# Kernel tuning notes

Measured on AMD Instinct MI355X. Metric: run time of the kernel, lower is better.

Reference implementation:

```python
import jax, jax.numpy as jnp
import numpy as np

D_MODEL = 1024
N_HEADS = 16
D_K = D_MODEL // N_HEADS
MAX_REL = 128
SCALE = 1.0 / np.sqrt(D_K)
TEMP = 1.0


def setup_inputs() -> dict:
    key = jax.random.key(0)
    ks = jax.random.split(key, 12)
    B, S = 4, 1024
    inp = {
        "query": jax.random.normal(ks[0], (B, S, D_MODEL), jnp.float32),
        "key": jax.random.normal(ks[1], (B, S, D_MODEL), jnp.float32),
        "value": jax.random.normal(ks[2], (B, S, D_MODEL), jnp.float32),
        "mask": jnp.ones((B, S), jnp.int32),
        "w_q": jax.random.normal(ks[3], (D_MODEL, D_MODEL), jnp.float32) * 0.03,
        "b_q": jnp.zeros((D_MODEL,), jnp.float32),
        "w_k": jax.random.normal(ks[4], (D_MODEL, D_MODEL), jnp.float32) * 0.03,
        "b_k": jnp.zeros((D_MODEL,), jnp.float32),
        "w_v": jax.random.normal(ks[5], (D_MODEL, D_MODEL), jnp.float32) * 0.03,
        "b_v": jnp.zeros((D_MODEL,), jnp.float32),
        "w_o": jax.random.normal(ks[6], (D_MODEL, D_MODEL), jnp.float32) * 0.03,
        "b_o": jnp.zeros((D_MODEL,), jnp.float32),
        "rel_k": jax.random.normal(ks[7], (2 * MAX_REL + 1, D_K), jnp.float32),
        "rel_v": jax.random.normal(ks[8], (2 * MAX_REL + 1, D_K), jnp.float32),
    }
    return inp


def _relative_positions(seq_len):
    pos = jnp.arange(seq_len)
    rel = pos[None, :] - pos[:, None]  # [S, S]
    return jnp.clip(rel, -MAX_REL, MAX_REL) + MAX_REL


def reference(query, key, value, mask, w_q, b_q, w_k, b_k, w_v, b_v, w_o, b_o, rel_k, rel_v):
    B, S, _ = query.shape
    # projections (torch Linear: x @ W.T + b)
    Q = (query @ w_q.T + b_q).reshape(B, S, N_HEADS, D_K).transpose(0, 2, 1, 3)  # [B,H,S,d]
    K = (key @ w_k.T + b_k).reshape(B, S, N_HEADS, D_K).transpose(0, 2, 1, 3)
    V = (value @ w_v.T + b_v).reshape(B, S, N_HEADS, D_K).transpose(0, 2, 1, 3)

    scores = jnp.einsum("bhld,bhrd->bhlr", Q, K) * SCALE  # [B,H,S,S]

    rel_idx = _relative_positions(S)                      # [S,S] int
    rpk = rel_k[rel_idx]                                  # [S,S,d]
    scores = scores + jnp.einsum("bhld,lrd->bhlr", Q, rpk)

    scores = scores / TEMP
    m = mask[:, None, None, :]                            # [B,1,1,S]
    scores = jnp.where(m == 0, -1e9, scores)

    attn = jax.nn.softmax(scores, axis=-1)                # [B,H,S,S]
    context = jnp.einsum("bhlr,bhrd->bhld", attn, V)
    rpv = rel_v[rel_idx]                                  # [S,S,d]
    context = context + jnp.einsum("bhlr,lrd->bhld", attn, rpv)

    context = context.transpose(0, 2, 1, 3).reshape(B, S, D_MODEL)
    out = context @ w_o.T + b_o
    return out
```

## Files before the change

### kernel.cpp

```cpp
#include <hip/hip_runtime.h>
#include <hip/hip_bf16.h>

#define S_LEN  1024
#define DMODEL 1024
#define NHEADS 16
#define DK     64
#define SCALE  0.125f

typedef __bf16 bf16x8_t __attribute__((ext_vector_type(8)));
typedef __bf16 bf16x4_t __attribute__((ext_vector_type(4)));
typedef float  f32x4_t  __attribute__((ext_vector_type(4)));

#define MFMA16(A, B, C) __builtin_amdgcn_mfma_f32_16x16x32_bf16((A), (B), (C), 0, 0, 0)

__device__ __forceinline__ void async16(const void* g, void* l) {
    __builtin_amdgcn_global_load_lds(
        (const __attribute__((address_space(1))) unsigned int*)g,
        (__attribute__((address_space(3))) unsigned int*)l, 16, 0, 0);
}

__global__ __launch_bounds__(256) void cast_all_kernel(
    const float* __restrict__ q, const float* __restrict__ k, const float* __restrict__ v,
    const float* __restrict__ wq, const float* __restrict__ wk,
    const float* __restrict__ wv, const float* __restrict__ wo,
    const float* __restrict__ relk, const float* __restrict__ relv,
    __bf16* __restrict__ Xbf, __bf16* __restrict__ Wall,
    __bf16* __restrict__ relkp, __bf16* __restrict__ rvT,
    __bf16* __restrict__ Wqlo)
{
    const long i = (long)blockIdx.x * 256 + threadIdx.x;
    if (i < 3145728) {
        const int z   = (int)(i >> 20);
        const long rem = i & 1048575;
        const float4 s = ((const float4*)(z == 0 ? q : (z == 1 ? k : v)))[rem];
        bf16x4_t h;
        h[0] = (__bf16)s.x; h[1] = (__bf16)s.y; h[2] = (__bf16)s.z; h[3] = (__bf16)s.w;
        *(bf16x4_t*)(Xbf + ((size_t)z << 22) + rem * 4) = h;
    } else if (i < 3145728 + 1048576) {
        const long wi = i - 3145728;
        const int z   = (int)(wi >> 18);
        const long rem = wi & 262143;
        const float* src = (z == 0) ? wq : (z == 1) ? wk : (z == 2) ? wv : wo;
        const float4 s = ((const float4*)src)[rem];
        const float xs[4] = {s.x, s.y, s.z, s.w};
        bf16x4_t h;
        #pragma unroll
        for (int t = 0; t < 4; ++t) h[t] = (__bf16)xs[t];
        *(bf16x4_t*)(Wall + ((size_t)z << 20) + rem * 4) = h;
        if (z == 0) {
            bf16x4_t l;
            #pragma unroll
            for (int t = 0; t < 4; ++t) l[t] = (__bf16)(xs[t] - (float)h[t]);
            *(bf16x4_t*)(Wqlo + rem * 4) = l;
        }
    } else if (i < 3145728 + 1048576 + 4352) {
        const long ri = i - (3145728 + 1048576);
        const int j  = (int)(ri >> 4);
        const int d4 = (int)(ri & 15) * 4;
        bf16x4_t h, l;
        if (j < 257) {
            const float4 s = *(const float4*)(relk + j * 64 + d4);
            const float xs[4] = {s.x, s.y, s.z, s.w};
            #pragma unroll
            for (int t = 0; t < 4; ++t) {
                h[t] = (__bf16)xs[t];
                l[t] = (__bf16)(xs[t] - (float)h[t]);
            }
        } else {
            #pragma unroll
            for (int t = 0; t < 4; ++t) { h[t] = (__bf16)0.f; l[t] = (__bf16)0.f; }
        }
        *(bf16x4_t*)(relkp + j * 64 + d4) = h;
        *(bf16x4_t*)(relkp + 17408 + j * 64 + d4) = l;
    } else if (i < 3145728 + 1048576 + 4352 + 4608) {
        const long ri = i - (3145728 + 1048576 + 4352);
        const int d  = (int)(ri / 72);
        const int j4 = (int)(ri % 72) * 4;
        bf16x4_t o;
        #pragma unroll
        for (int t = 0; t < 4; ++t) {
            const int j = j4 + t;
            o[t] = (j < 257) ? (__bf16)relv[j * 64 + d] : (__bf16)0.f;
        }
        *(bf16x4_t*)(rvT + d * 288 + j4) = o;
    }
}

__device__ __forceinline__ void gemm128_core(
    const __bf16* __restrict__ A, const __bf16* __restrict__ W,
    __bf16* As, __bf16* Ws, f32x4_t acc[4][4])
{
    const int tid  = threadIdx.x;
    const int lane = tid & 63;
    const int quad = lane >> 4;
    const int l15  = lane & 15;
    const int wid  = tid >> 6;
    const int wm = wid >> 1, wn = wid & 1;

    for (int kt = 0; kt < 32; ++kt) {
        #pragma unroll
        for (int r = 0; r < 2; ++r) {
            const int c = r * 256 + tid;
            const int row = c >> 2, kb = c & 3;
            async16(A + row * 1024 + kt * 32 + kb * 8, As + c * 8);
            async16(W + row * 1024 + kt * 32 + kb * 8, Ws + c * 8);
        }
        __syncthreads();
        bf16x8_t af[4], wf[4];
        #pragma unroll
        for (int i = 0; i < 4; ++i) {
            af[i] = *(const bf16x8_t*)(As + (wm * 64 + i * 16 + l15) * 32 + quad * 8);
            wf[i] = *(const bf16x8_t*)(Ws + (wn * 64 + i * 16 + l15) * 32 + quad * 8);
        }
        #pragma unroll
        for (int i = 0; i < 4; ++i)
            #pragma unroll
            for (int j = 0; j < 4; ++j)
                acc[i][j] = MFMA16(af[i], wf[j], acc[i][j]);
        __syncthreads();
    }
}

__global__ __launch_bounds__(256) void gemm_qkv_kernel(
    const __bf16* __restrict__ Xbf, const __bf16* __restrict__ Wall,
    const __bf16* __restrict__ Wqlo,
    const float* __restrict__ bq, const float* __restrict__ bk, const float* __restrict__ bv,
    __bf16* __restrict__ QKVh)
{
    __shared__ __bf16 As[4096], Ws[4096];
    const int z = blockIdx.z;
    const __bf16* A = Xbf + (size_t)z * 4194304 + (size_t)blockIdx.y * 131072;
    const __bf16* W = Wall + (size_t)z * 1048576 + (size_t)blockIdx.x * 131072;
    f32x4_t acc[4][4];
    #pragma unroll
    for (int i = 0; i < 4; ++i)
        #pragma unroll
        for (int j = 0; j < 4; ++j)
            acc[i][j] = (f32x4_t){0.f, 0.f, 0.f, 0.f};

    gemm128_core(A, W, As, Ws, acc);
    if (z == 0)
        gemm128_core(A, Wqlo + (size_t)blockIdx.x * 131072, As, Ws, acc);

    const int tid = threadIdx.x, lane = tid & 63, quad = lane >> 4, l15 = lane & 15;
    const int wid = tid >> 6, wm = wid >> 1, wn = wid & 1;
    const int m0 = blockIdx.y * 128 + wm * 64;
    const int n0 = blockIdx.x * 128 + wn * 64;
    const float* bias = (z == 0) ? bq : ((z == 1) ? bk : bv);
    __bf16* dst = QKVh + (size_t)z * 4194304;

    if (z < 2) {
        #pragma unroll
        for (int j = 0; j < 4; ++j) {
            const int n = n0 + j * 16 + l15;
            const float bn = bias[n];
            #pragma unroll
            for (int i = 0; i < 4; ++i) {
                #pragma unroll
                for (int v = 0; v < 4; ++v) {
                    const int m = m0 + i * 16 + quad * 4 + v;
                    dst[((((m >> 10) * 16 + (n >> 6)) << 16)) + ((m & 1023) << 6) + (n & 63)]
                        = (__bf16)(acc[i][j][v] + bn);
                }
            }
        }
    } else {
        #pragma unroll
        for (int j = 0; j < 4; ++j) {
            const int n = n0 + j * 16 + l15;
            const float bn = bias[n];
            #pragma unroll
            for (int i = 0; i < 4; ++i) {
                const int m = m0 + i * 16 + quad * 4;
                bf16x4_t pk;
                #pragma unroll
                for (int v = 0; v < 4; ++v) pk[v] = (__bf16)(acc[i][j][v] + bn);
                const int s = m & 1023, d = n & 63;
                const size_t idx = (((size_t)((m >> 10) * 16 + (n >> 6))) << 16)
                                 + (size_t)(s >> 5) * 2048 + d * 32 + (s & 31);
                *(bf16x4_t*)(dst + idx) = pk;
            }
        }
    }
}

__global__ __launch_bounds__(256) void gemm_out_kernel(
    const __bf16* __restrict__ ctx, const __bf16* __restrict__ Wo,
    const float* __restrict__ bo, float* __restrict__ out)
{
    __shared__ __bf16 As[4096], Ws[4096];
    const __bf16* A = ctx + (size_t)blockIdx.y * 131072;
    const __bf16* W = Wo + (size_t)blockIdx.x * 131072;
    f32x4_t acc[4][4];
    #pragma unroll
    for (int i = 0; i < 4; ++i)
        #pragma unroll
        for (int j = 0; j < 4; ++j)
            acc[i][j] = (f32x4_t){0.f, 0.f, 0.f, 0.f};
    gemm128_core(A, W, As, Ws, acc);

    const int tid = threadIdx.x, lane = tid & 63, quad = lane >> 4, l15 = lane & 15;
    const int wid = tid >> 6, wm = wid >> 1, wn = wid & 1;
    const int m0 = blockIdx.y * 128 + wm * 64;
    const int n0 = blockIdx.x * 128 + wn * 64;
    #pragma unroll
    for (int j = 0; j < 4; ++j) {
        const int n = n0 + j * 16 + l15;
        const float bn = bo[n];
        #pragma unroll
        for (int i = 0; i < 4; ++i)
            #pragma unroll
            for (int v = 0; v < 4; ++v) {
                const int m = m0 + i * 16 + quad * 4 + v;
                out[(size_t)m * 1024 + n] = acc[i][j][v] + bn;
            }
    }
}

__global__ __launch_bounds__(128, 2) void attn_fused_kernel(
    const __bf16* __restrict__ Qh, const __bf16* __restrict__ Kh,
    const __bf16* __restrict__ Vt, const __bf16* __restrict__ relkp,
    const __bf16* __restrict__ rvT, const int* __restrict__ mask,
    const float* __restrict__ relv, __bf16* __restrict__ ctx)
{
    __shared__ __align__(16) __bf16 Ks[2][2048];
    __shared__ __align__(16) __bf16 Vs[2][2048];
    __shared__ __align__(16) __bf16 p_s[2][16][40];
    __shared__ __align__(16) __bf16 w_s[2][16][272];

    const int tid = threadIdx.x, lane = tid & 63, wid = tid >> 6;
    const int quad = lane >> 4, l15 = lane & 15;
    const int lin = blockIdx.x;
    const int slot = lin >> 3;
    const int bh = (lin & 7) + 8 * (slot >> 5);
    const int chunk = slot & 31;
    const int b = bh >> 4;
    const int t0w = chunk * 2 + wid;
    const int l0 = t0w * 16;

    const __bf16* Qbase = Qh + (size_t)bh * 65536;
    const __bf16* Kbase = Kh + (size_t)bh * 65536;
    const __bf16* Vbase = Vt + (size_t)bh * 65536;
    const int* maskb = mask + b * 1024;
    const __bf16* rlo = relkp + 17408;

    int gK[4], lK[4], gV[4], lV[4];
    #pragma unroll
    for (int ii = 0; ii < 4; ++ii) {
        const int ch = ii * 64 + lane;
        {
            const int r = ch >> 3, p = ch & 7, g = p ^ (r & 7);
            gK[ii] = r * 64 + g * 8;
            lK[ii] = ch * 8;
        }
        {
            const int d = ch >> 2, p = ch & 3, g = p ^ ((d >> 1) & 3);
            gV[ii] = d * 32 + g * 8;
            lV[ii] = ch * 8;
        }
    }

    if (wid == 0) {
        #pragma unroll
        for (int ii = 0; ii < 4; ++ii)
            async16(Kbase + gK[ii], &Ks[0][0] + lK[ii]);
    } else {
        #pragma unroll
        for (int ii = 0; ii < 4; ++ii)
            async16(Vbase + gV[ii], &Vs[0][0] + lV[ii]);
    }

    const bf16x8_t aq0 = *(const bf16x8_t*)(Qbase + (l0 + l15) * 64 + quad * 8);
    const bf16x8_t aq1 = *(const bf16x8_t*)(Qbase + (l0 + l15) * 64 + 32 + quad * 8);

    float c0[4], c1[4];
    {
        const int jr = (l15 == 1) ? 256 : 0;
        const bf16x8_t bh0 = *(const bf16x8_t*)(relkp + jr * 64 + quad * 8);
        const bf16x8_t bh1 = *(const bf16x8_t*)(relkp + jr * 64 + 32 + quad * 8);
        const bf16x8_t bl0 = *(const bf16x8_t*)(rlo + jr * 64 + quad * 8);
        const bf16x8_t bl1 = *(const bf16x8_t*)(rlo + jr * 64 + 32 + quad * 8);
        f32x4_t cr = (f32x4_t){0.f, 0.f, 0.f, 0.f};
        cr = MFMA16(aq0, bl0, cr);
        cr = MFMA16(aq1, bl1, cr);
        cr = MFMA16(aq0, bh0, cr);
        cr = MFMA16(aq1, bh1, cr);
        #pragma unroll
        for (int v = 0; v < 4; ++v) {
            c0[v] = __shfl(cr[v], (lane & 48), 64);
            c1[v] = __shfl(cr[v], (lane & 48) | 1, 64);
        }
    }

    {
        uint4* wz = (uint4*)&w_s[wid][0][0];
        for (int t = lane; t < 544; t += 64) wz[t] = (uint4){0u, 0u, 0u, 0u};
    }

    f32x4_t o[4];
    #pragma unroll
    for (int dt = 0; dt < 4; ++dt) o[dt] = (f32x4_t){0.f, 0.f, 0.f, 0.f};
    float rowsum[4] = {0.f, 0.f, 0.f, 0.f};
    float e0[4] = {0.f, 0.f, 0.f, 0.f};
    float e1[4] = {0.f, 0.f, 0.f, 0.f};

    __syncthreads();

    for (int pc = 0; pc < 32; ++pc) {
        const int cur = pc & 1;
        if (pc + 1 < 32) {
            if (wid == 0) {
                #pragma unroll
                for (int ii = 0; ii < 4; ++ii)
                    async16(Kbase + (pc + 1) * 2048 + gK[ii], &Ks[cur ^ 1][0] + lK[ii]);
            } else {
                #pragma unroll
                for (int ii = 0; ii < 4; ++ii)
                    async16(Vbase + (pc + 1) * 2048 + gV[ii], &Vs[cur ^ 1][0] + lV[ii]);
            }
        }

        const int rb0 = pc * 32;
        const int tI0 = pc * 2;
        #pragma unroll
        for (int sl = 0; sl < 2; ++sl) {
            const int tI = tI0 + sl;
            const int dist = tI - t0w;
            const int R = sl * 16 + l15;
            const bf16x8_t kb0 =
                *(const bf16x8_t*)(&Ks[cur][0] + R * 64 + (quad ^ (R & 7)) * 8);
            const bf16x8_t kb1 =
                *(const bf16x8_t*)(&Ks[cur][0] + R * 64 + (((quad + 4) ^ (R & 7))) * 8);
            f32x4_t s = (f32x4_t){0.f, 0.f, 0.f, 0.f};
            s = MFMA16(aq0, kb0, s);
            s = MFMA16(aq1, kb1, s);
            const float madd = (maskb[rb0 + R] == 0) ? -1.0e9f : 0.f;

            if (dist <= -9 || dist >= 9) {
                const bool isLo = dist < 0;
                #pragma unroll
                for (int v = 0; v < 4; ++v) {
                    const float cc = isLo ? c0[v] : c1[v];
                    const float p = __expf(fmaf(s[v], SCALE, cc) + madd);
                    const __bf16 pb = (__bf16)p;
                    const float pf = (float)pb;
                    rowsum[v] += pf;
                    if (isLo) e0[v] += pf; else e1[v] += pf;
                    p_s[wid][quad * 4 + v][sl * 16 + l15] = pb;
                }
            } else {
                const int base = dist * 16 + 128;
                int ra = base - 15 + l15;
                ra = ra < 0 ? 0 : (ra > 256 ? 256 : ra);
                int rb2 = base + 1 + l15;
                rb2 = rb2 > 256 ? 256 : rb2;
                const bf16x8_t hA0 = *(const bf16x8_t*)(relkp + ra * 64 + quad * 8);
                const bf16x8_t hA1 = *(const bf16x8_t*)(relkp + ra * 64 + 32 + quad * 8);
                const bf16x8_t lA0 = *(const bf16x8_t*)(rlo + ra * 64 + quad * 8);
                const bf16x8_t lA1 = *(const bf16x8_t*)(rlo + ra * 64 + 32 + quad * 8);
                const bf16x8_t hB0 = *(const bf16x8_t*)(relkp + rb2 * 64 + quad * 8);
                const bf16x8_t hB1 = *(const bf16x8_t*)(relkp + rb2 * 64 + 32 + quad * 8);
                const bf16x8_t lB0 = *(const bf16x8_t*)(rlo + rb2 * 64 + quad * 8);
                const bf16x8_t lB1 = *(const bf16x8_t*)(rlo + rb2 * 64 + 32 + quad * 8);
                f32x4_t qbA = (f32x4_t){0.f, 0.f, 0.f, 0.f};
                f32x4_t qbB = (f32x4_t){0.f, 0.f, 0.f, 0.f};
                qbA = MFMA16(aq0, lA0, qbA);
                qbA = MFMA16(aq1, lA1, qbA);
                qbA = MFMA16(aq0, hA0, qbA);
                qbA = MFMA16(aq1, hA1, qbA);
                qbB = MFMA16(aq0, lB0, qbB);
                qbB = MFMA16(aq1, lB1, qbB);
                qbB = MFMA16(aq0, hB0, qbB);
                qbB = MFMA16(aq1, hB1, qbB);
                #pragma unroll
                for (int v = 0; v < 4; ++v) {
                    const int lrow = quad * 4 + v;
                    const int c = l15 + 15 - lrow;
                    const int src = (lane & 48) | (c & 15);
                    const float bA = __shfl(qbA[v], src, 64);
                    const float bB = __shfl(qbB[v], src, 64);
                    const float qbv = (c & 16) ? bB : bA;
                    const int j = base + l15 - lrow;
                    const float bias = (j < 0) ? c0[v] : ((j > 256) ? c1[v] : qbv);
                    const float p = __expf(fmaf(s[v], SCALE, bias) + madd);
                    const __bf16 pb = (__bf16)p;
                    const float pf = (float)pb;
                    rowsum[v] += pf;
                    p_s[wid][lrow][sl * 16 + l15] = pb;
                    if (j <= 0)        e0[v] += pf;
                    else if (j >= 256) e1[v] += pf;
                    else               w_s[wid][lrow][j] = pb;
                }
            }
        }
        const bf16x8_t pa = *(const bf16x8_t*)(&p_s[wid][l15][quad * 8]);
        #pragma unroll
        for (int dt = 0; dt < 4; ++dt) {
            const int D = dt * 16 + l15;
            const bf16x8_t vb =
                *(const bf16x8_t*)(&Vs[cur][0] + D * 32 + ((quad ^ ((D >> 1) & 3))) * 8);
            o[dt] = MFMA16(pa, vb, o[dt]);
        }
        __syncthreads();
    }

    for (int kc = 0; kc < 8; ++kc) {
        const bf16x8_t wa = *(const bf16x8_t*)(&w_s[wid][l15][kc * 32 + quad * 8]);
        #pragma unroll
        for (int dt = 0; dt < 4; ++dt) {
            const bf16x8_t rb =
                *(const bf16x8_t*)(rvT + (dt * 16 + l15) * 288 + kc * 32 + quad * 8);
            o[dt] = MFMA16(wa, rb, o[dt]);
        }
    }

    #pragma unroll
    for (int v = 0; v < 4; ++v) {
        #pragma unroll
        for (int mm = 1; mm < 16; mm <<= 1) {
            rowsum[v] += __shfl_xor(rowsum[v], mm, 64);
            e0[v]     += __shfl_xor(e0[v], mm, 64);
            e1[v]     += __shfl_xor(e1[v], mm, 64);
        }
    }

    float rinv[4];
    #pragma unroll
    for (int v = 0; v < 4; ++v)
        rinv[v] = 1.f / rowsum[v];
    const int h = bh & 15;
    #pragma unroll
    for (int dt = 0; dt < 4; ++dt) {
        const int d = dt * 16 + l15;
        const float rv0   = relv[d];
        const float rv256 = relv[256 * 64 + d];
        #pragma unroll
        for (int v = 0; v < 4; ++v) {
            const int lrow = quad * 4 + v;
            const float val = (o[dt][v] + e0[v] * rv0 + e1[v] * rv256) * rinv[v];
            ctx[((size_t)b * 1024 + l0 + lrow) * 1024 + h * 64 + d] = (__bf16)val;
        }
    }
}

extern "C" void kernel_launch(void* const* d_in, const int* in_sizes, int n_in,
                              void* d_out, int out_size, void* d_ws, size_t ws_size,
                              hipStream_t stream)
{
    const float* q    = (const float*)d_in[0];
    const float* k    = (const float*)d_in[1];
    const float* v    = (const float*)d_in[2];
    const int*   mask = (const int*)  d_in[3];
    const float* wq   = (const float*)d_in[4];
    const float* bq   = (const float*)d_in[5];
    const float* wk   = (const float*)d_in[6];
    const float* bk   = (const float*)d_in[7];
    const float* wv   = (const float*)d_in[8];
    const float* bv   = (const float*)d_in[9];
    const float* wo   = (const float*)d_in[10];
    const float* bo   = (const float*)d_in[11];
    const float* relk = (const float*)d_in[12];
    const float* relv = (const float*)d_in[13];

    __bf16* Xbf   = (__bf16*)d_ws;
    __bf16* Xgap  = Xbf   + 12582912;
    __bf16* Wqlo  = Xgap  + 4194304;
    __bf16* Wall  = Wqlo  + 1048576;
    __bf16* QKVh  = Wall  + 4194304;
    __bf16* ctx   = QKVh  + 12582912;
    __bf16* relkp = ctx   + 4194304;
    __bf16* rvT   = relkp + 34816;

    cast_all_kernel<<<16419, 256, 0, stream>>>(q, k, v, wq, wk, wv, wo, relk, relv,
                                               Xbf, Wall, relkp, rvT, Wqlo);
    gemm_qkv_kernel<<<dim3(8, 32, 3), 256, 0, stream>>>(Xbf, Wall, Wqlo,
                                                        bq, bk, bv, QKVh);
    attn_fused_kernel<<<2048, 128, 0, stream>>>(QKVh, QKVh + 4194304,
                                                QKVh + 2 * 4194304, relkp,
                                                rvT, mask, relv, ctx);
    gemm_out_kernel<<<dim3(8, 32, 1), 256, 0, stream>>>(ctx, Wall + 3 * 1048576,
                                                        bo, (float*)d_out);
}
```

Before: 340.8 us.

## Use 4-wave attention blocks, triple-buffer K/V, and carry relative-key bias tiles

The attention kernel now runs 4 waves per block over 64 query rows, so each K/V tile loaded into LDS is shared by twice as many waves. K/V staging goes from double to triple buffering, with two tiles in flight, explicit vmcnt waits and a single barrier per iteration in place of the trailing __syncthreads. In the near-diagonal path, the upper relative-key bias MFMA result from one tile is carried over as the lower half for the next, which removes four MFMAs and four global loads in most band tiles. The risks are lower occupancy from more LDS per block and correctness hazards from the hand-written waitcnt and barrier ordering.

After: 305.8 us. 1.11x faster.

```diff
diff --git a/kernel.cpp b/kernel.cpp
--- a/kernel.cpp
+++ b/kernel.cpp
@@ -217,25 +217,25 @@
     }
 }
 
-__global__ __launch_bounds__(128, 2) void attn_fused_kernel(
+__global__ __launch_bounds__(256, 2) void attn_fused_kernel(
     const __bf16* __restrict__ Qh, const __bf16* __restrict__ Kh,
     const __bf16* __restrict__ Vt, const __bf16* __restrict__ relkp,
     const __bf16* __restrict__ rvT, const int* __restrict__ mask,
     const float* __restrict__ relv, __bf16* __restrict__ ctx)
 {
-    __shared__ __align__(16) __bf16 Ks[2][2048];
-    __shared__ __align__(16) __bf16 Vs[2][2048];
-    __shared__ __align__(16) __bf16 p_s[2][16][40];
-    __shared__ __align__(16) __bf16 w_s[2][16][272];
+    __shared__ __align__(16) __bf16 Ks[3][2048];
+    __shared__ __align__(16) __bf16 Vs[3][2048];
+    __shared__ __align__(16) __bf16 p_s[4][16][40];
+    __shared__ __align__(16) __bf16 w_s[4][16][264];
 
     const int tid = threadIdx.x, lane = tid & 63, wid = tid >> 6;
     const int quad = lane >> 4, l15 = lane & 15;
     const int lin = blockIdx.x;
     const int slot = lin >> 3;
-    const int bh = (lin & 7) + 8 * (slot >> 5);
-    const int chunk = slot & 31;
+    const int bh = (lin & 7) + 8 * (slot >> 4);
+    const int chunk = slot & 15;
     const int b = bh >> 4;
-    const int t0w = chunk * 2 + wid;
+    const int t0w = chunk * 4 + wid;
     const int l0 = t0w * 16;
 
     const __bf16* Qbase = Qh + (size_t)bh * 65536;
@@ -244,31 +244,32 @@
     const int* maskb = mask + b * 1024;
     const __bf16* rlo = relkp + 17408;
 
-    int gK[4], lK[4], gV[4], lV[4];
-    #pragma unroll
-    for (int ii = 0; ii < 4; ++ii) {
-        const int ch = ii * 64 + lane;
-        {
-            const int r = ch >> 3, p = ch & 7, g = p ^ (r & 7);
-            gK[ii] = r * 64 + g * 8;
-            lK[ii] = ch * 8;
-        }
-        {
-            const int d = ch >> 2, p = ch & 3, g = p ^ ((d >> 1) & 3);
-            gV[ii] = d * 32 + g * 8;
-            lV[ii] = ch * 8;
-        }
-    }
-
-    if (wid == 0) {
-        #pragma unroll
-        for (int ii = 0; ii < 4; ++ii)
-            async16(Kbase + gK[ii], &Ks[0][0] + lK[ii]);
-    } else {
-        #pragma unroll
-        for (int ii = 0; ii < 4; ++ii)
-            async16(Vbase + gV[ii], &Vs[0][0] + lV[ii]);
-    }
+    int gKo[2], lKo[2], gVo[2], lVo[2];
+    #pragma unroll
+    for (int ii = 0; ii < 2; ++ii) {
+        const int chK = (wid & 1) * 128 + ii * 64 + lane;
+        const int rK = chK >> 3, pK = chK & 7, gK = pK ^ (rK & 7);
+        gKo[ii] = rK * 64 + gK * 8;
+        lKo[ii] = chK * 8;
+        const int chV = (wid & 1) * 128 + ii * 64 + lane;
+        const int dV = chV >> 2, pV = chV & 3, gV = pV ^ ((dV >> 1) & 3);
+        gVo[ii] = dV * 32 + gV * 8;
+        lVo[ii] = chV * 8;
+    }
+
+    #define STAGE(t, buf)                                                     \
+        do {                                                                  \
+            if (wid < 2) {                                                    \
+                async16(Kbase + (t) * 2048 + gKo[0], &Ks[buf][0] + lKo[0]);   \
+                async16(Kbase + (t) * 2048 + gKo[1], &Ks[buf][0] + lKo[1]);   \
+            } else {                                                          \
+                async16(Vbase + (t) * 2048 + gVo[0], &Vs[buf][0] + lVo[0]);   \
+                async16(Vbase + (t) * 2048 + gVo[1], &Vs[buf][0] + lVo[1]);   \
+            }                                                                 \
+        } while (0)
+
+    STAGE(0, 0);
+    STAGE(1, 1);
 
     const bf16x8_t aq0 = *(const bf16x8_t*)(Qbase + (l0 + l15) * 64 + quad * 8);
     const bf16x8_t aq1 = *(const bf16x8_t*)(Qbase + (l0 + l15) * 64 + 32 + quad * 8);
@@ -294,7 +295,7 @@
 
     {
         uint4* wz = (uint4*)&w_s[wid][0][0];
-        for (int t = lane; t < 544; t += 64) wz[t] = (uint4){0u, 0u, 0u, 0u};
+        for (int t = lane; t < 528; t += 64) wz[t] = (uint4){0u, 0u, 0u, 0u};
     }
 
     f32x4_t o[4];
@@ -303,23 +304,17 @@
     float rowsum[4] = {0.f, 0.f, 0.f, 0.f};
     float e0[4] = {0.f, 0.f, 0.f, 0.f};
     float e1[4] = {0.f, 0.f, 0.f, 0.f};
-
-    __syncthreads();
+    f32x4_t qb_carry = (f32x4_t){0.f, 0.f, 0.f, 0.f};
 
     for (int pc = 0; pc < 32; ++pc) {
-        const int cur = pc & 1;
-        if (pc + 1 < 32) {
-            if (wid == 0) {
-                #pragma unroll
-                for (int ii = 0; ii < 4; ++ii)
-                    async16(Kbase + (pc + 1) * 2048 + gK[ii], &Ks[cur ^ 1][0] + lK[ii]);
-            } else {
-                #pragma unroll
-                for (int ii = 0; ii < 4; ++ii)
-                    async16(Vbase + (pc + 1) * 2048 + gV[ii], &Vs[cur ^ 1][0] + lV[ii]);
-            }
-        }
-
+        if (pc < 31) asm volatile("s_waitcnt vmcnt(2)" ::: "memory");
+        else         asm volatile("s_waitcnt vmcnt(0)" ::: "memory");
+        asm volatile("" ::: "memory");
+        __builtin_amdgcn_s_barrier();
+        asm volatile("" ::: "memory");
+        if (pc + 2 < 32) STAGE(pc + 2, (pc + 2) % 3);
+
+        const int cur = pc % 3;
         const int rb0 = pc * 32;
         const int tI0 = pc * 2;
         #pragma unroll
@@ -350,28 +345,35 @@
                 }
             } else {
                 const int base = dist * 16 + 128;
-                int ra = base - 15 + l15;
-                ra = ra < 0 ? 0 : (ra > 256 ? 256 : ra);
+                f32x4_t qbA;
+                const bool seed = (dist == -8) || (tI == 0);
+                if (seed) {
+                    int ra = base - 15 + l15;
+                    ra = ra < 0 ? 0 : (ra > 256 ? 256 : ra);
+                    const bf16x8_t hA0 = *(const bf16x8_t*)(relkp + ra * 64 + quad * 8);
+                    const bf16x8_t hA1 = *(const bf16x8_t*)(relkp + ra * 64 + 32 + quad * 8);
+                    const bf16x8_t lA0 = *(const bf16x8_t*)(rlo + ra * 64 + quad * 8);
+                    const bf16x8_t lA1 = *(const bf16x8_t*)(rlo + ra * 64 + 32 + quad * 8);
+                    qbA = (f32x4_t){0.f, 0.f, 0.f, 0.f};
+                    qbA = MFMA16(aq0, lA0, qbA);
+                    qbA = MFMA16(aq1, lA1, qbA);
+                    qbA = MFMA16(aq0, hA0, qbA);
+                    qbA = MFMA16(aq1, hA1, qbA);
+                } else {
+                    qbA = qb_carry;
+                }
                 int rb2 = base + 1 + l15;
                 rb2 = rb2 > 256 ? 256 : rb2;
-                const bf16x8_t hA0 = *(const bf16x8_t*)(relkp + ra * 64 + quad * 8);
-                const bf16x8_t hA1 = *(const bf16x8_t*)(relkp + ra * 64 + 32 + quad * 8);
-                const bf16x8_t lA0 = *(const bf16x8_t*)(rlo + ra * 64 + quad * 8);
-                const bf16x8_t lA1 = *(const bf16x8_t*)(rlo + ra * 64 + 32 + quad * 8);
                 const bf16x8_t hB0 = *(const bf16x8_t*)(relkp + rb2 * 64 + quad * 8);
                 const bf16x8_t hB1 = *(const bf16x8_t*)(relkp + rb2 * 64 + 32 + quad * 8);
                 const bf16x8_t lB0 = *(const bf16x8_t*)(rlo + rb2 * 64 + quad * 8);
                 const bf16x8_t lB1 = *(const bf16x8_t*)(rlo + rb2 * 64 + 32 + quad * 8);
-                f32x4_t qbA = (f32x4_t){0.f, 0.f, 0.f, 0.f};
                 f32x4_t qbB = (f32x4_t){0.f, 0.f, 0.f, 0.f};
-                qbA = MFMA16(aq0, lA0, qbA);
-                qbA = MFMA16(aq1, lA1, qbA);
-                qbA = MFMA16(aq0, hA0, qbA);
-                qbA = MFMA16(aq1, hA1, qbA);
                 qbB = MFMA16(aq0, lB0, qbB);
                 qbB = MFMA16(aq1, lB1, qbB);
                 qbB = MFMA16(aq0, hB0, qbB);
                 qbB = MFMA16(aq1, hB1, qbB);
+                qb_carry = qbB;
                 #pragma unroll
                 for (int v = 0; v < 4; ++v) {
                     const int lrow = quad * 4 + v;
@@ -401,8 +403,8 @@
                 *(const bf16x8_t*)(&Vs[cur][0] + D * 32 + ((quad ^ ((D >> 1) & 3))) * 8);
             o[dt] = MFMA16(pa, vb, o[dt]);
         }
-        __syncthreads();
-    }
+    }
+    #undef STAGE
 
     for (int kc = 0; kc < 8; ++kc) {
         const bf16x8_t wa = *(const bf16x8_t*)(&w_s[wid][l15][kc * 32 + quad * 8]);
@@ -475,7 +477,7 @@
                                                Xbf, Wall, relkp, rvT, Wqlo);
     gemm_qkv_kernel<<<dim3(8, 32, 3), 256, 0, stream>>>(Xbf, Wall, Wqlo,
                                                         bq, bk, bv, QKVh);
-    attn_fused_kernel<<<2048, 128, 0, stream>>>(QKVh, QKVh + 4194304,
+    attn_fused_kernel<<<1024, 256, 0, stream>>>(QKVh, QKVh + 4194304,
                                                 QKVh + 2 * 4194304, relkp,
                                                 rvT, mask, relv, ctx);
     gemm_out_kernel<<<dim3(8, 32, 1), 256, 0, stream>>>(ctx, Wall + 3 * 1048576,
```
